# Optimization experiments

Measured on AMD Instinct MI355X. Metric: run time of the kernel, lower is better.

Reference implementation:

```python
import jax, jax.numpy as jnp
import numpy as np

H = 8; DH = 32; MAX_HOP = 256; NUM_EDGE = 25
NHOP = MAX_HOP + 2   # 258 (incl. UNREACHABLE)
NEDGE = NUM_EDGE + 2 # 27  (incl. NO_EDGE)


def _ln(x, g, b, eps=1e-5):
    m = x.mean(-1, keepdims=True)
    v = ((x - m) ** 2).mean(-1, keepdims=True)
    return (x - m) / jnp.sqrt(v + eps) * g + b


def _scatter_bins(att, idx, M):
    # att: [B,H,N,N] probs, idx: [B,N,N] int bins -> [B,H,N,M] scatter-add over keys
    B, Hh, N, _ = att.shape
    idxb = jnp.broadcast_to(idx[:, None, :, :], att.shape)
    bi = jnp.arange(B)[:, None, None, None]
    hi = jnp.arange(Hh)[None, :, None, None]
    ni = jnp.arange(N)[None, None, :, None]
    return jnp.zeros((B, Hh, N, M), att.dtype).at[bi, hi, ni, idxb].add(att)


def _forward(x, mask, distance_mat, edge_attr_mat,
             node_W, node_b, ln1_g, ln1_b, Wq, bq, Wk, bk, Wv, bv, Wo, bo,
             ln2_g, ln2_b, W1, b1, W2, b2,
             q_hop, q_edge, k_hop, k_edge, v_hop, v_edge,
             fln_g, fln_b, out_W, out_b):
    B, N, _ = x.shape
    h = x @ node_W + node_b  # [B,N,DM]
    # index preprocessing (clamp then -1 -> sentinel, as in torch)
    dist = jnp.minimum(distance_mat, MAX_HOP)
    dist = jnp.where(dist == -1, MAX_HOP + 1, dist)
    edge = jnp.minimum(edge_attr_mat, NUM_EDGE)
    edge = jnp.where(edge == -1, NUM_EDGE + 1, edge)

    # ---- encoder layer ----
    y = _ln(h, ln1_g, ln1_b)
    q = (y @ Wq + bq).reshape(B, N, H, DH).transpose(0, 2, 1, 3)  # bhnd
    k = (y @ Wk + bk).reshape(B, N, H, DH).transpose(0, 2, 1, 3)
    v = (y @ Wv + bv).reshape(B, N, H, DH).transpose(0, 2, 1, 3)
    Qh = q_hop.reshape(NHOP, H, DH).transpose(1, 0, 2)   # [H,M,d]
    Qe = q_edge.reshape(NEDGE, H, DH).transpose(1, 0, 2)
    Kh = k_hop.reshape(NHOP, H, DH).transpose(1, 0, 2)
    Ke = k_edge.reshape(NEDGE, H, DH).transpose(1, 0, 2)
    Vh = v_hop.reshape(NHOP, H, DH).transpose(1, 0, 2)
    Ve = v_edge.reshape(NEDGE, H, DH).transpose(1, 0, 2)

    dist_b = jnp.broadcast_to(dist[:, None, :, :], (B, H, N, N))
    edge_b = jnp.broadcast_to(edge[:, None, :, :], (B, H, N, N))

    qh = jnp.einsum('bhnd,hmd->bhnm', q, Qh)  # [B,H,N,M]
    query_hop = jnp.take_along_axis(qh, dist_b, axis=3)
    qe = jnp.einsum('bhnd,hmd->bhnm', q, Qe)
    query_edge = jnp.take_along_axis(qe, edge_b, axis=3)
    kh = jnp.einsum('bhnd,hmd->bhnm', k, Kh)
    # torch gathers along dim 2 of kh^T: key_hop[b,h,i,j] = k_j . Kh[dist[i,j]]
    key_hop = jnp.take_along_axis(jnp.swapaxes(kh, 2, 3), dist_b, axis=2)
    ke = jnp.einsum('bhnd,hmd->bhnm', k, Ke)
    key_edge = jnp.take_along_axis(ke, edge_b, axis=3)

    scale = DH ** (-0.5)
    scores = (jnp.einsum('bhid,bhjd->bhij', q, k)
              + (query_hop + key_hop) + (query_edge + key_edge)) * scale
    scores = jnp.where(mask[:, None, None, :], -jnp.inf, scores)
    att = jax.nn.softmax(scores, axis=-1)

    vha = _scatter_bins(att, dist, NHOP)   # [B,H,N,NHOP]
    vea = _scatter_bins(att, edge, NEDGE)
    ctx = (jnp.einsum('bhij,bhjd->bhid', att, v)
           + jnp.einsum('bhim,hmd->bhid', vha, Vh)
           + jnp.einsum('bhim,hmd->bhid', vea, Ve))
    ctx = ctx.transpose(0, 2, 1, 3).reshape(B, N, H * DH)
    h = h + (ctx @ Wo + bo)

    y = _ln(h, ln2_g, ln2_b)
    y = jax.nn.gelu(y @ W1 + b1, approximate=False) @ W2 + b2
    h = h + y
    # ---- head ----
    out = _ln(h, fln_g, fln_b)
    return out @ out_W + out_b


def setup_inputs() -> dict:
    key = jax.random.key(0)
    ks = jax.random.split(key, 40)
    D_IN, DM, FF, OUT, B, N = 128, 256, 1024, 128, 16, 512
    nrm = lambda k, shape, s=0.02: jax.random.normal(k, shape, jnp.float32) * s
    z = lambda shape: jnp.zeros(shape, jnp.float32)
    o = lambda shape: jnp.ones(shape, jnp.float32)
    return {
        'x': jax.random.normal(ks[0], (B, N, D_IN), jnp.float32),
        'mask': jnp.zeros((B, N), bool),
        'distance_mat': jax.random.randint(ks[1], (B, N, N), 0, 257),
        'edge_attr_mat': jax.random.randint(ks[2], (B, N, N), 0, 26),
        'node_W': nrm(ks[3], (D_IN, DM)), 'node_b': z((DM,)),
        'ln1_g': o((DM,)), 'ln1_b': z((DM,)),
        'Wq': nrm(ks[4], (DM, DM)), 'bq': z((DM,)),
        'Wk': nrm(ks[5], (DM, DM)), 'bk': z((DM,)),
        'Wv': nrm(ks[6], (DM, DM)), 'bv': z((DM,)),
        'Wo': nrm(ks[7], (DM, DM)), 'bo': z((DM,)),
        'ln2_g': o((DM,)), 'ln2_b': z((DM,)),
        'W1': nrm(ks[8], (DM, FF)), 'b1': z((FF,)),
        'W2': nrm(ks[9], (FF, DM)), 'b2': z((DM,)),
        'q_hop': nrm(ks[10], (NHOP, DM)), 'q_edge': nrm(ks[11], (NEDGE, DM)),
        'k_hop': nrm(ks[12], (NHOP, DM)), 'k_edge': nrm(ks[13], (NEDGE, DM)),
        'v_hop': nrm(ks[14], (NHOP, DM)), 'v_edge': nrm(ks[15], (NEDGE, DM)),
        'fln_g': o((DM,)), 'fln_b': z((DM,)),
        'out_W': nrm(ks[16], (DM, OUT)), 'out_b': z((OUT,)),
    }


def reference(x, mask, distance_mat, edge_attr_mat,
              node_W, node_b, ln1_g, ln1_b, Wq, bq, Wk, bk, Wv, bv, Wo, bo,
              ln2_g, ln2_b, W1, b1, W2, b2,
              q_hop, q_edge, k_hop, k_edge, v_hop, v_edge,
              fln_g, fln_b, out_W, out_b):
    return _forward(x, mask, distance_mat, edge_attr_mat,
                    node_W, node_b, ln1_g, ln1_b, Wq, bq, Wk, bk, Wv, bv, Wo, bo,
                    ln2_g, ln2_b, W1, b1, W2, b2,
                    q_hop, q_edge, k_hop, k_edge, v_hop, v_edge,
                    fln_g, fln_b, out_W, out_b)
```

## Files before the change

kernel.cpp:

```cpp
#include <hip/hip_runtime.h>
#include <hip/hip_bf16.h>
#include <math.h>

#define BB 16
#define NN 512
#define DIN 128
#define DM 256
#define NH 8
#define DH 32
#define FF 1024
#define DOUT 128
#define NHOP 258
#define NEDGE 27
#define ROWS (BB*NN)
#define QHE_S 296

typedef short short8 __attribute__((ext_vector_type(8)));
typedef float f32x4 __attribute__((ext_vector_type(4)));

static __device__ __forceinline__ float bf2f(unsigned short u) {
    union { float f; unsigned int i; } c; c.i = ((unsigned int)u) << 16; return c.f;
}
static __device__ __forceinline__ short f2bs(float f) {
    __hip_bfloat16 h = __float2bfloat16(f);
    return *reinterpret_cast<short*>(&h);
}

__global__ __launch_bounds__(256) void k_ln(const float* __restrict__ in, const float* __restrict__ g,
                                            const float* __restrict__ bta, float* __restrict__ out) {
    int row = blockIdx.x * 4 + (threadIdx.x >> 6);
    int l = threadIdx.x & 63;
    float4 xv = ((const float4*)(in + (size_t)row*DM))[l];
    float s = xv.x + xv.y + xv.z + xv.w;
    #pragma unroll
    for (int o = 32; o > 0; o >>= 1) s += __shfl_xor(s, o, 64);
    float mean = s * (1.0f/DM);
    float dx = xv.x-mean, dy = xv.y-mean, dz = xv.z-mean, dw = xv.w-mean;
    float vs = dx*dx + dy*dy + dz*dz + dw*dw;
    #pragma unroll
    for (int o = 32; o > 0; o >>= 1) vs += __shfl_xor(vs, o, 64);
    float r = rsqrtf(vs * (1.0f/DM) + 1e-5f);
    float4 gg = ((const float4*)g)[l];
    float4 bb = ((const float4*)bta)[l];
    float4 ov; ov.x = dx*r*gg.x+bb.x; ov.y = dy*r*gg.y+bb.y; ov.z = dz*r*gg.z+bb.z; ov.w = dw*r*gg.w+bb.w;
    ((float4*)(out + (size_t)row*DM))[l] = ov;
}

template<int K, int N, int ACT, int RES, int QKV>
__global__ __launch_bounds__(256) void k_mgemm(const float* __restrict__ A, const float* __restrict__ W,
                                               const float* __restrict__ bias, float* __restrict__ out) {
    __shared__ __align__(16) short As[64][40];
    __shared__ __align__(16) short Bs[64][40];
    int r0 = blockIdx.x * 64;
    int n0 = blockIdx.y * 64;
    int tid = threadIdx.x;
    int w = tid >> 6, l = tid & 63;

    f32x4 acc[4];
    #pragma unroll
    for (int c = 0; c < 4; ++c) acc[c] = (f32x4){0.f,0.f,0.f,0.f};

    for (int k0 = 0; k0 < K; k0 += 32) {
        __syncthreads();
        {
            int m = tid >> 2, ks = (tid & 3) * 8;
            const float* src = A + (size_t)(r0 + m)*K + k0 + ks;
            float4 f0 = *(const float4*)src;
            float4 f1 = *(const float4*)(src + 4);
            short8 pk;
            pk[0]=f2bs(f0.x); pk[1]=f2bs(f0.y); pk[2]=f2bs(f0.z); pk[3]=f2bs(f0.w);
            pk[4]=f2bs(f1.x); pk[5]=f2bs(f1.y); pk[6]=f2bs(f1.z); pk[7]=f2bs(f1.w);
            *(short8*)&As[m][ks] = pk;
        }
        {
            int n = tid & 63, kg = tid >> 6;
            const float* wp = W + (size_t)(k0 + kg*8)*N + n0 + n;
            short8 pk;
            #pragma unroll
            for (int j = 0; j < 8; ++j) pk[j] = f2bs(wp[(size_t)j*N]);
            *(short8*)&Bs[n][kg*8] = pk;
        }
        __syncthreads();
        short8 af = *(short8*)&As[w*16 + (l & 15)][(l >> 4)*8];
        #pragma unroll
        for (int c = 0; c < 4; ++c) {
            short8 bf = *(short8*)&Bs[c*16 + (l & 15)][(l >> 4)*8];
            acc[c] = __builtin_amdgcn_mfma_f32_16x16x32_bf16(af, bf, acc[c], 0, 0, 0);
        }
    }

    int quad = l >> 4;
    #pragma unroll
    for (int c = 0; c < 4; ++c) {
        int col = n0 + c*16 + (l & 15);
        float bv = bias[col];
        #pragma unroll
        for (int reg = 0; reg < 4; ++reg) {
            int row = r0 + w*16 + quad*4 + reg;
            float val = acc[c][reg] + bv;
            if (ACT) val = 0.5f * val * (1.0f + erff(val * 0.70710678118654752f));
            if (QKV) {
                int b = row >> 9, n = row & (NN-1);
                int hh = col >> 5, d = col & (DH-1);
                out[(size_t)((b*NH + hh)*NN + n)*DH + d] = val;
            } else if (RES) {
                out[(size_t)row*N + col] += val;
            } else {
                out[(size_t)row*N + col] = val;
            }
        }
    }
}

__global__ __launch_bounds__(256) void k_tr(const float* __restrict__ in, float* __restrict__ out, int M) {
    int m = blockIdx.x, t = threadIdx.x;
    out[((size_t)(t >> 5)*M + m)*DH + (t & 31)] = in[(size_t)m*DM + t];
}

__global__ __launch_bounds__(256) void k_trd(const float* __restrict__ in, float* __restrict__ out, int M) {
    int m = blockIdx.x, t = threadIdx.x;
    out[(size_t)t*M + m] = in[(size_t)m*DM + t];
}

__global__ __launch_bounds__(256) void k_tx(const float* __restrict__ k, float* __restrict__ kT) {
    __shared__ float lds[64*33];
    int bh = blockIdx.x;
    int j0 = blockIdx.y * 64;
    int tid = threadIdx.x;
    {
        int jj = tid >> 2, d8 = tid & 3;
        const float* src = k + ((size_t)bh*NN + j0 + jj)*DH + d8*8;
        float4 a = *(const float4*)(src);
        float4 b = *(const float4*)(src + 4);
        float* dst = lds + jj*33 + d8*8;
        dst[0]=a.x; dst[1]=a.y; dst[2]=a.z; dst[3]=a.w;
        dst[4]=b.x; dst[5]=b.y; dst[6]=b.z; dst[7]=b.w;
    }
    __syncthreads();
    {
        int d = tid >> 3, jg = tid & 7;
        float* dst = kT + ((size_t)bh*DH + d)*NN + j0;
        #pragma unroll
        for (int jj2 = 0; jj2 < 8; ++jj2) {
            int j = jg*8 + jj2;
            dst[j] = lds[j*33 + d];
        }
    }
}

__global__ __launch_bounds__(256) void k_kht(const float* __restrict__ kT, const float* __restrict__ k_hop,
                                             __hip_bfloat16* __restrict__ kht) {
    int bm = blockIdx.x;
    int m = bm % NHOP;
    int bh = bm / NHOP;
    int hh = bh & (NH-1);
    float kh[32];
    {
        const float4* khp = (const float4*)(k_hop + (size_t)m*DM + hh*DH);
        #pragma unroll
        for (int c = 0; c < 8; ++c) *(float4*)&kh[c*4] = khp[c];
    }
    const float* kTb = kT + (size_t)bh*DH*NN;
    #pragma unroll
    for (int it = 0; it < 2; ++it) {
        int j = threadIdx.x + it*256;
        float acc = 0.f;
        #pragma unroll
        for (int d = 0; d < DH; ++d) acc += kh[d] * kTb[(size_t)d*NN + j];
        kht[(size_t)bm*NN + j] = __float2bfloat16(acc);
    }
}

__global__ __launch_bounds__(256) void k_qhe(const float* __restrict__ q, const float* __restrict__ k,
                                             const float* __restrict__ Qh_d, const float* __restrict__ Qe_d,
                                             const float* __restrict__ Ke_d, unsigned short* __restrict__ qhe) {
    int bh = blockIdx.x;
    int hh = bh & (NH-1);
    int i0 = blockIdx.y * 16;
    int tid = threadIdx.x;
    __shared__ __align__(16) float As[16][32];
    __shared__ __align__(16) float Ks[16][32];
    {
        int r = (tid & 127) >> 3, c4 = tid & 7;
        const float* src = ((tid < 128) ? q : k) + ((size_t)bh*NN + i0 + r)*DH + c4*4;
        float4 vv = *(const float4*)src;
        float* dst = (tid < 128) ? &As[r][c4*4] : &Ks[r][c4*4];
        *(float4*)dst = vv;
    }
    __syncthreads();
    {
        float acc[16];
        #pragma unroll
        for (int r = 0; r < 16; ++r) acc[r] = 0.f;
        const float* wb = Qh_d + (size_t)hh*32*NHOP + tid;
        for (int d = 0; d < 32; ++d) {
            float wv = wb[(size_t)d*NHOP];
            #pragma unroll
            for (int r = 0; r < 16; ++r) acc[r] += As[r][d] * wv;
        }
        #pragma unroll
        for (int r = 0; r < 16; ++r) {
            __hip_bfloat16 bv = __float2bfloat16(acc[r]);
            qhe[((size_t)bh*NN + i0 + r)*QHE_S + tid] = *(unsigned short*)&bv;
        }
    }
    if (tid < 2) {
        int m = 256 + tid;
        float acc[16];
        #pragma unroll
        for (int r = 0; r < 16; ++r) acc[r] = 0.f;
        const float* wb = Qh_d + (size_t)hh*32*NHOP + m;
        for (int d = 0; d < 32; ++d) {
            float wv = wb[(size_t)d*NHOP];
            #pragma unroll
            for (int r = 0; r < 16; ++r) acc[r] += As[r][d] * wv;
        }
        #pragma unroll
        for (int r = 0; r < 16; ++r) {
            __hip_bfloat16 bv = __float2bfloat16(acc[r]);
            qhe[((size_t)bh*NN + i0 + r)*QHE_S + m] = *(unsigned short*)&bv;
        }
    } else if (tid >= 8 && tid < 8 + NEDGE) {
        int e = tid - 8;
        float acc[16];
        #pragma unroll
        for (int r = 0; r < 16; ++r) acc[r] = 0.f;
        const float* wq = Qe_d + (size_t)hh*32*NEDGE + e;
        const float* wk = Ke_d + (size_t)hh*32*NEDGE + e;
        for (int d = 0; d < 32; ++d) {
            float a = wq[(size_t)d*NEDGE], bbw = wk[(size_t)d*NEDGE];
            #pragma unroll
            for (int r = 0; r < 16; ++r) acc[r] += As[r][d]*a + Ks[r][d]*bbw;
        }
        #pragma unroll
        for (int r = 0; r < 16; ++r) {
            __hip_bfloat16 bv = __float2bfloat16(acc[r]);
            qhe[((size_t)bh*NN + i0 + r)*QHE_S + 264 + e] = *(unsigned short*)&bv;
        }
    }
}

__global__ __launch_bounds__(512) void k_attn(
    const float* __restrict__ q, const float* __restrict__ kT, const float* __restrict__ v,
    const __hip_bfloat16* __restrict__ kht, const int* __restrict__ dist, const int* __restrict__ edge,
    const unsigned char* __restrict__ mask, const unsigned short* __restrict__ qhe,
    const float* __restrict__ Vh_t, const float* __restrict__ Ve_t,
    float* __restrict__ ctx)
{
    int g  = blockIdx.x;
    int rr = g >> 3;
    int b  = (g & 7) + ((rr >> 7) << 3);
    int i0 = (rr & 127) * 4;
    int w  = threadIdx.x >> 6;
    int l  = threadIdx.x & 63;
    int bh = b*NH + w;

    __shared__ unsigned short mje[4][NN];
    __shared__ float qv[NH][4][DH];
    __shared__ __hip_bfloat16 pb[NH][4][NN];
    __shared__ float bins[NH][292];

    {
        int t = threadIdx.x;
        int row = t >> 7, c4 = t & 127;
        int4 dv = ((const int4*)(dist + ((size_t)(b*NN) + i0 + row)*NN))[c4];
        int4 ev = ((const int4*)(edge + ((size_t)(b*NN) + i0 + row)*NN))[c4];
        int m0 = dv.x > 256 ? 256 : dv.x; if (dv.x < 0) m0 = 257;
        int m1 = dv.y > 256 ? 256 : dv.y; if (dv.y < 0) m1 = 257;
        int m2 = dv.z > 256 ? 256 : dv.z; if (dv.z < 0) m2 = 257;
        int m3 = dv.w > 256 ? 256 : dv.w; if (dv.w < 0) m3 = 257;
        int e0 = ev.x > 25 ? 25 : ev.x; if (ev.x < 0) e0 = 26;
        int e1 = ev.y > 25 ? 25 : ev.y; if (ev.y < 0) e1 = 26;
        int e2 = ev.z > 25 ? 25 : ev.z; if (ev.z < 0) e2 = 26;
        int e3 = ev.w > 25 ? 25 : ev.w; if (ev.w < 0) e3 = 26;
        mje[row][c4*4+0] = (unsigned short)(m0 | (e0 << 9));
        mje[row][c4*4+1] = (unsigned short)(m1 | (e1 << 9));
        mje[row][c4*4+2] = (unsigned short)(m2 | (e2 << 9));
        mje[row][c4*4+3] = (unsigned short)(m3 | (e3 << 9));
        #pragma unroll
        for (int rep = 0; rep < 2; ++rep) {
            int i = rep*2 + (l >> 5), d = l & 31;
            qv[w][i][d] = q[((size_t)bh*NN + i0 + i)*DH + d];
        }
        for (int s = l; s < 292; s += 64) bins[w][s] = 0.f;
    }
    __syncthreads();

    float sc[4][8];
    #pragma unroll
    for (int i = 0; i < 4; ++i)
        #pragma unroll
        for (int s = 0; s < 8; ++s) sc[i][s] = 0.f;
    {
        const float* kTb = kT + (size_t)bh*DH*NN;
        for (int d = 0; d < 32; ++d) {
            const float* kr = kTb + (size_t)d*NN + l;
            float k0 = kr[0],   k1 = kr[64],  k2 = kr[128], k3 = kr[192];
            float k4 = kr[256], k5 = kr[320], k6 = kr[384], k7 = kr[448];
            float qa = qv[w][0][d], qb = qv[w][1][d], qc = qv[w][2][d], qd = qv[w][3][d];
            sc[0][0]+=qa*k0; sc[0][1]+=qa*k1; sc[0][2]+=qa*k2; sc[0][3]+=qa*k3;
            sc[0][4]+=qa*k4; sc[0][5]+=qa*k5; sc[0][6]+=qa*k6; sc[0][7]+=qa*k7;
            sc[1][0]+=qb*k0; sc[1][1]+=qb*k1; sc[1][2]+=qb*k2; sc[1][3]+=qb*k3;
            sc[1][4]+=qb*k4; sc[1][5]+=qb*k5; sc[1][6]+=qb*k6; sc[1][7]+=qb*k7;
            sc[2][0]+=qc*k0; sc[2][1]+=qc*k1; sc[2][2]+=qc*k2; sc[2][3]+=qc*k3;
            sc[2][4]+=qc*k4; sc[2][5]+=qc*k5; sc[2][6]+=qc*k6; sc[2][7]+=qc*k7;
            sc[3][0]+=qd*k0; sc[3][1]+=qd*k1; sc[3][2]+=qd*k2; sc[3][3]+=qd*k3;
            sc[3][4]+=qd*k4; sc[3][5]+=qd*k5; sc[3][6]+=qd*k6; sc[3][7]+=qd*k7;
        }
    }

    const __hip_bfloat16* khtb = kht + (size_t)bh*NHOP*NN;
    const unsigned char* mrow = mask + (size_t)b*NN;
    unsigned char msk[8];
    #pragma unroll
    for (int s = 0; s < 8; ++s) msk[s] = mrow[l + 64*s];

    int jc = l >> 3, d4 = l & 7;
    const float* vhb = Vh_t + (size_t)w*NHOP*DH + d4*4;
    const float* veb = Ve_t + (size_t)w*NEDGE*DH + d4*4;
    const float scale = 0.17677669529663687f;
    float4 acc[4];

    #pragma unroll
    for (int i = 0; i < 4; ++i) {
        const unsigned short* qhr = qhe + ((size_t)bh*NN + i0 + i)*QHE_S;
        int mv[8], ev[8];
        #pragma unroll
        for (int s = 0; s < 8; ++s) { int pk = mje[i][l + 64*s]; mv[s] = pk & 511; ev[s] = pk >> 9; }
        unsigned short raw[8];
        #pragma unroll
        for (int s = 0; s < 8; ++s) raw[s] = ((const unsigned short*)khtb)[(size_t)mv[s]*NN + l + 64*s];
        unsigned short qhv[8], qev[8];
        #pragma unroll
        for (int s = 0; s < 8; ++s) qhv[s] = qhr[mv[s]];
        #pragma unroll
        for (int s = 0; s < 8; ++s) qev[s] = qhr[264 + ev[s]];
        float x[8];
        #pragma unroll
        for (int s = 0; s < 8; ++s) {
            float a = (sc[i][s] + bf2f(qhv[s]) + bf2f(raw[s]) + bf2f(qev[s])) * scale;
            if (msk[s]) a = -INFINITY;
            x[s] = a;
        }
        float mx = x[0];
        #pragma unroll
        for (int s = 1; s < 8; ++s) mx = fmaxf(mx, x[s]);
        #pragma unroll
        for (int o = 32; o > 0; o >>= 1) mx = fmaxf(mx, __shfl_xor(mx, o, 64));
        float sum = 0.f;
        #pragma unroll
        for (int s = 0; s < 8; ++s) { x[s] = __expf(x[s] - mx); sum += x[s]; }
        #pragma unroll
        for (int o = 32; o > 0; o >>= 1) sum += __shfl_xor(sum, o, 64);
        float inv = 1.0f / sum;
        #pragma unroll
        for (int s = 0; s < 8; ++s) {
            float ps = x[s] * inv;
            pb[w][i][l + 64*s] = __float2bfloat16(ps);
            atomicAdd(&bins[w][mv[s]], ps);
            atomicAdd(&bins[w][264 + ev[s]], ps);
        }
        float4 a4; a4.x = a4.y = a4.z = a4.w = 0.f;
        for (int t = 0; t < 33; ++t) {
            int m = 8*t + jc;
            if (m < NHOP) {
                float bw = bins[w][m];
                float4 vv = *(const float4*)(vhb + (size_t)m*DH);
                a4.x += bw*vv.x; a4.y += bw*vv.y; a4.z += bw*vv.z; a4.w += bw*vv.w;
            }
        }
        #pragma unroll
        for (int t = 0; t < 4; ++t) {
            int e = 8*t + jc;
            if (e < NEDGE) {
                float bw = bins[w][264 + e];
                float4 vv = *(const float4*)(veb + (size_t)e*DH);
                a4.x += bw*vv.x; a4.y += bw*vv.y; a4.z += bw*vv.z; a4.w += bw*vv.w;
            }
        }
        acc[i] = a4;
        if (i < 3) {
            for (int s2 = l; s2 < 292; s2 += 64) bins[w][s2] = 0.f;
        }
    }

    {
        const float* vb = v + (size_t)bh*NN*DH + d4*4;
        for (int off = 0; off < 64; ++off) {
            int j = 8*off + jc;
            float4 vv = *(const float4*)(vb + (size_t)j*DH);
            #pragma unroll
            for (int i = 0; i < 4; ++i) {
                float p = bf2f(*(const unsigned short*)&pb[w][i][j]);
                acc[i].x += p*vv.x; acc[i].y += p*vv.y; acc[i].z += p*vv.z; acc[i].w += p*vv.w;
            }
        }
    }
    #pragma unroll
    for (int i = 0; i < 4; ++i) {
        #pragma unroll
        for (int o = 8; o <= 32; o <<= 1) {
            acc[i].x += __shfl_xor(acc[i].x, o, 64);
            acc[i].y += __shfl_xor(acc[i].y, o, 64);
            acc[i].z += __shfl_xor(acc[i].z, o, 64);
            acc[i].w += __shfl_xor(acc[i].w, o, 64);
        }
        if (jc == 0) {
            *(float4*)(ctx + ((size_t)b*NN + i0 + i)*DM + w*DH + d4*4) = acc[i];
        }
    }
}

extern "C" void kernel_launch(void* const* d_in, const int* in_sizes, int n_in,
                              void* d_out, int out_size, void* d_ws, size_t ws_size,
                              hipStream_t stream) {
    const float* x     = (const float*)d_in[0];
    const unsigned char* mask = (const unsigned char*)d_in[1];
    const int*   dist  = (const int*)d_in[2];
    const int*   edge  = (const int*)d_in[3];
    const float* node_W = (const float*)d_in[4];
    const float* node_b = (const float*)d_in[5];
    const float* ln1_g = (const float*)d_in[6];
    const float* ln1_b = (const float*)d_in[7];
    const float* Wq = (const float*)d_in[8];
    const float* bq = (const float*)d_in[9];
    const float* Wk = (const float*)d_in[10];
    const float* bk = (const float*)d_in[11];
    const float* Wv = (const float*)d_in[12];
    const float* bv = (const float*)d_in[13];
    const float* Wo = (const float*)d_in[14];
    const float* bo = (const float*)d_in[15];
    const float* ln2_g = (const float*)d_in[16];
    const float* ln2_b = (const float*)d_in[17];
    const float* W1 = (const float*)d_in[18];
    const float* b1 = (const float*)d_in[19];
    const float* W2 = (const float*)d_in[20];
    const float* b2 = (const float*)d_in[21];
    const float* q_hop  = (const float*)d_in[22];
    const float* q_edge = (const float*)d_in[23];
    const float* k_hop  = (const float*)d_in[24];
    const float* k_edge = (const float*)d_in[25];
    const float* v_hop  = (const float*)d_in[26];
    const float* v_edge = (const float*)d_in[27];
    const float* fln_g = (const float*)d_in[28];
    const float* fln_b = (const float*)d_in[29];
    const float* out_W = (const float*)d_in[30];
    const float* out_b = (const float*)d_in[31];
    float* out = (float*)d_out;

    float* ws = (float*)d_ws;
    float* h   = ws + 0;
    float* y   = ws + 2097152;
    float* q   = ws + 4194304;
    float* k   = ws + 6291456;
    float* v   = ws + 8388608;
    float* ctx = ws + 10485760;
    __hip_bfloat16* kht = (__hip_bfloat16*)(ws + 12582912);
    float* ffn = ws + 12582912;
    float* kT  = ws + 21037056;
    unsigned short* qhe = (unsigned short*)(ws + 23134208);
    float* Vh_t = y + 0;
    float* Ve_t = y + 66048;
    float* Qh_d = y + 72960;
    float* Qe_d = y + 139008;
    float* Ke_d = y + 145920;

    k_mgemm<DIN, DM, 0, 0, 0><<<dim3(ROWS/64, DM/64), 256, 0, stream>>>(x, node_W, node_b, h);
    k_ln<<<ROWS/4, 256, 0, stream>>>(h, ln1_g, ln1_b, y);
    k_mgemm<DM, DM, 0, 0, 1><<<dim3(ROWS/64, DM/64), 256, 0, stream>>>(y, Wq, bq, q);
    k_mgemm<DM, DM, 0, 0, 1><<<dim3(ROWS/64, DM/64), 256, 0, stream>>>(y, Wk, bk, k);
    k_mgemm<DM, DM, 0, 0, 1><<<dim3(ROWS/64, DM/64), 256, 0, stream>>>(y, Wv, bv, v);
    k_tr <<<NHOP, 256, 0, stream>>>(v_hop, Vh_t, NHOP);
    k_tr <<<NEDGE, 256, 0, stream>>>(v_edge, Ve_t, NEDGE);
    k_trd<<<NHOP, 256, 0, stream>>>(q_hop, Qh_d, NHOP);
    k_trd<<<NEDGE, 256, 0, stream>>>(q_edge, Qe_d, NEDGE);
    k_trd<<<NEDGE, 256, 0, stream>>>(k_edge, Ke_d, NEDGE);
    k_tx<<<dim3(BB*NH, 8), 256, 0, stream>>>(k, kT);
    k_kht<<<BB*NH*NHOP, 256, 0, stream>>>(kT, k_hop, kht);
    k_qhe<<<dim3(BB*NH, NN/16), 256, 0, stream>>>(q, k, Qh_d, Qe_d, Ke_d, qhe);
    k_attn<<<BB*(NN/4), 512, 0, stream>>>(q, kT, v, kht, dist, edge, mask, qhe,
                                          Vh_t, Ve_t, ctx);
    k_mgemm<DM, DM, 0, 1, 0><<<dim3(ROWS/64, DM/64), 256, 0, stream>>>(ctx, Wo, bo, h);
    k_ln<<<ROWS/4, 256, 0, stream>>>(h, ln2_g, ln2_b, y);
    k_mgemm<DM, FF, 1, 0, 0><<<dim3(ROWS/64, FF/64), 256, 0, stream>>>(y, W1, b1, ffn);
    k_mgemm<FF, DM, 0, 1, 0><<<dim3(ROWS/64, DM/64), 256, 0, stream>>>(ffn, W2, b2, h);
    k_ln<<<ROWS/4, 256, 0, stream>>>(h, fln_g, fln_b, y);
    k_mgemm<DM, DOUT, 0, 0, 0><<<dim3(ROWS/64, DOUT/64), 256, 0, stream>>>(y, out_W, out_b, out);
}
```

Before: 873.2 us.

## Split attention into score kernel and separate bin-value GEMV kernel

The fused attention kernel is split in two. The score kernel now runs 4 heads per 256-thread block instead of 8 heads per 512-thread block, and it writes the per-row hop/edge bin probabilities as bf16 into the qhe buffer, overwriting its now-consumed entries. A new k_av kernel then multiplies those bins by a combined, zero-padded transposed Vh/Ve table and adds the result into ctx. This moves the scattered per-row float4 loads of the hop and edge value tables out of the softmax kernel and cuts its LDS use, at the cost of an extra launch, a global round-trip for the bins, and bf16 rounding of the bin weights.

```diff
diff --git a/kernel.cpp b/kernel.cpp
--- a/kernel.cpp
+++ b/kernel.cpp
@@ -112,14 +112,19 @@
     }
 }
 
-__global__ __launch_bounds__(256) void k_tr(const float* __restrict__ in, float* __restrict__ out, int M) {
-    int m = blockIdx.x, t = threadIdx.x;
-    out[((size_t)(t >> 5)*M + m)*DH + (t & 31)] = in[(size_t)m*DM + t];
-}
-
 __global__ __launch_bounds__(256) void k_trd(const float* __restrict__ in, float* __restrict__ out, int M) {
     int m = blockIdx.x, t = threadIdx.x;
     out[(size_t)t*M + m] = in[(size_t)m*DM + t];
+}
+
+__global__ __launch_bounds__(256) void k_vhve(const float* __restrict__ vh, const float* __restrict__ ve,
+                                              float* __restrict__ out) {
+    int m = blockIdx.x;
+    int t = threadIdx.x;
+    float val = 0.f;
+    if (m < NHOP) val = vh[(size_t)m*DM + t];
+    else if (m >= 264 && m < 264 + NEDGE) val = ve[(size_t)(m - 264)*DM + t];
+    out[((size_t)(t >> 5)*QHE_S + m)*DH + (t & 31)] = val;
 }
 
 __global__ __launch_bounds__(256) void k_tx(const float* __restrict__ k, float* __restrict__ kT) {
@@ -199,10 +204,8 @@
             for (int r = 0; r < 16; ++r) acc[r] += As[r][d] * wv;
         }
         #pragma unroll
-        for (int r = 0; r < 16; ++r) {
-            __hip_bfloat16 bv = __float2bfloat16(acc[r]);
-            qhe[((size_t)bh*NN + i0 + r)*QHE_S + tid] = *(unsigned short*)&bv;
-        }
+        for (int r = 0; r < 16; ++r)
+            qhe[((size_t)bh*NN + i0 + r)*QHE_S + tid] = (unsigned short)f2bs(acc[r]);
     }
     if (tid < 2) {
         int m = 256 + tid;
@@ -216,10 +219,8 @@
             for (int r = 0; r < 16; ++r) acc[r] += As[r][d] * wv;
         }
         #pragma unroll
-        for (int r = 0; r < 16; ++r) {
-            __hip_bfloat16 bv = __float2bfloat16(acc[r]);
-            qhe[((size_t)bh*NN + i0 + r)*QHE_S + m] = *(unsigned short*)&bv;
-        }
+        for (int r = 0; r < 16; ++r)
+            qhe[((size_t)bh*NN + i0 + r)*QHE_S + m] = (unsigned short)f2bs(acc[r]);
     } else if (tid >= 8 && tid < 8 + NEDGE) {
         int e = tid - 8;
         float acc[16];
@@ -233,50 +234,54 @@
             for (int r = 0; r < 16; ++r) acc[r] += As[r][d]*a + Ks[r][d]*bbw;
         }
         #pragma unroll
-        for (int r = 0; r < 16; ++r) {
-            __hip_bfloat16 bv = __float2bfloat16(acc[r]);
-            qhe[((size_t)bh*NN + i0 + r)*QHE_S + 264 + e] = *(unsigned short*)&bv;
-        }
-    }
-}
-
-__global__ __launch_bounds__(512) void k_attn(
+        for (int r = 0; r < 16; ++r)
+            qhe[((size_t)bh*NN + i0 + r)*QHE_S + 264 + e] = (unsigned short)f2bs(acc[r]);
+    }
+}
+
+__global__ __launch_bounds__(256) void k_score(
     const float* __restrict__ q, const float* __restrict__ kT, const float* __restrict__ v,
     const __hip_bfloat16* __restrict__ kht, const int* __restrict__ dist, const int* __restrict__ edge,
-    const unsigned char* __restrict__ mask, const unsigned short* __restrict__ qhe,
-    const float* __restrict__ Vh_t, const float* __restrict__ Ve_t,
+    const unsigned char* __restrict__ mask, unsigned short* __restrict__ qhe,
     float* __restrict__ ctx)
 {
-    int g  = blockIdx.x;
-    int rr = g >> 3;
-    int b  = (g & 7) + ((rr >> 7) << 3);
-    int i0 = (rr & 127) * 4;
-    int w  = threadIdx.x >> 6;
-    int l  = threadIdx.x & 63;
-    int bh = b*NH + w;
+    int g   = blockIdx.x;
+    int r   = g >> 3;
+    int b   = (g & 7) + ((r >> 8) << 3);
+    int rem = r & 255;
+    int i0  = (rem >> 1) * 4;
+    int hg  = rem & 1;
+    int w   = threadIdx.x >> 6;
+    int l   = threadIdx.x & 63;
+    int hh  = hg*4 + w;
+    int bh  = b*NH + hh;
 
     __shared__ unsigned short mje[4][NN];
-    __shared__ float qv[NH][4][DH];
-    __shared__ __hip_bfloat16 pb[NH][4][NN];
-    __shared__ float bins[NH][292];
+    __shared__ float qv[4][4][DH];
+    __shared__ __hip_bfloat16 pb[4][4][NN];
+    __shared__ float bins[4][292];
 
     {
         int t = threadIdx.x;
-        int row = t >> 7, c4 = t & 127;
-        int4 dv = ((const int4*)(dist + ((size_t)(b*NN) + i0 + row)*NN))[c4];
-        int4 ev = ((const int4*)(edge + ((size_t)(b*NN) + i0 + row)*NN))[c4];
-        int m0 = dv.x > 256 ? 256 : dv.x; if (dv.x < 0) m0 = 257;
-        int m1 = dv.y > 256 ? 256 : dv.y; if (dv.y < 0) m1 = 257;
-        int m2 = dv.z > 256 ? 256 : dv.z; if (dv.z < 0) m2 = 257;
-        int m3 = dv.w > 256 ? 256 : dv.w; if (dv.w < 0) m3 = 257;
-        int e0 = ev.x > 25 ? 25 : ev.x; if (ev.x < 0) e0 = 26;
-        int e1 = ev.y > 25 ? 25 : ev.y; if (ev.y < 0) e1 = 26;
-        int e2 = ev.z > 25 ? 25 : ev.z; if (ev.z < 0) e2 = 26;
-        int e3 = ev.w > 25 ? 25 : ev.w; if (ev.w < 0) e3 = 26;
-        mje[row][c4*4+0] = (unsigned short)(m0 | (e0 << 9));
-        mje[row][c4*4+1] = (unsigned short)(m1 | (e1 << 9));
-        mje[row][c4*4+2] = (unsigned short)(m2 | (e2 << 9));
-        mje[row][c4*4+3] = (unsigned short)(m3 | (e3 << 9));
+        int row = t >> 6, c0 = t & 63;
+        #pragma unroll
+        for (int rep = 0; rep < 2; ++rep) {
+            int c4 = c0 + rep*64;
+            int4 dv = ((const int4*)(dist + ((size_t)(b*NN) + i0 + row)*NN))[c4];
+            int4 ev = ((const int4*)(edge + ((size_t)(b*NN) + i0 + row)*NN))[c4];
+            int m0 = dv.x > 256 ? 256 : dv.x; if (dv.x < 0) m0 = 257;
+            int m1 = dv.y > 256 ? 256 : dv.y; if (dv.y < 0) m1 = 257;
+            int m2 = dv.z > 256 ? 256 : dv.z; if (dv.z < 0) m2 = 257;
+            int m3 = dv.w > 256 ? 256 : dv.w; if (dv.w < 0) m3 = 257;
+            int e0 = ev.x > 25 ? 25 : ev.x; if (ev.x < 0) e0 = 26;
+            int e1 = ev.y > 25 ? 25 : ev.y; if (ev.y < 0) e1 = 26;
+            int e2 = ev.z > 25 ? 25 : ev.z; if (ev.z < 0) e2 = 26;
+            int e3 = ev.w > 25 ? 25 : ev.w; if (ev.w < 0) e3 = 26;
+            mje[row][c4*4+0] = (unsigned short)(m0 | (e0 << 9));
+            mje[row][c4*4+1] = (unsigned short)(m1 | (e1 << 9));
+            mje[row][c4*4+2] = (unsigned short)(m2 | (e2 << 9));
+            mje[row][c4*4+3] = (unsigned short)(m3 | (e3 << 9));
+        }
         #pragma unroll
         for (int rep = 0; rep < 2; ++rep) {
             int i = rep*2 + (l >> 5), d = l & 31;
@@ -314,27 +319,23 @@
     unsigned char msk[8];
     #pragma unroll
     for (int s = 0; s < 8; ++s) msk[s] = mrow[l + 64*s];
-
-    int jc = l >> 3, d4 = l & 7;
-    const float* vhb = Vh_t + (size_t)w*NHOP*DH + d4*4;
-    const float* veb = Ve_t + (size_t)w*NEDGE*DH + d4*4;
     const float scale = 0.17677669529663687f;
-    float4 acc[4];
 
     #pragma unroll
     for (int i = 0; i < 4; ++i) {
-        const unsigned short* qhr = qhe + ((size_t)bh*NN + i0 + i)*QHE_S;
-        int mv[8], ev[8];
-        #pragma unroll
-        for (int s = 0; s < 8; ++s) { int pk = mje[i][l + 64*s]; mv[s] = pk & 511; ev[s] = pk >> 9; }
+        unsigned short* qhr = qhe + ((size_t)bh*NN + i0 + i)*QHE_S;
+        int pk[8];
+        #pragma unroll
+        for (int s = 0; s < 8; ++s) pk[s] = mje[i][l + 64*s];
         unsigned short raw[8];
         #pragma unroll
-        for (int s = 0; s < 8; ++s) raw[s] = ((const unsigned short*)khtb)[(size_t)mv[s]*NN + l + 64*s];
+        for (int s = 0; s < 8; ++s)
+            raw[s] = ((const unsigned short*)khtb)[(size_t)(pk[s] & 511)*NN + l + 64*s];
         unsigned short qhv[8], qev[8];
         #pragma unroll
-        for (int s = 0; s < 8; ++s) qhv[s] = qhr[mv[s]];
-        #pragma unroll
-        for (int s = 0; s < 8; ++s) qev[s] = qhr[264 + ev[s]];
+        for (int s = 0; s < 8; ++s) qhv[s] = qhr[pk[s] & 511];
+        #pragma unroll
+        for (int s = 0; s < 8; ++s) qev[s] = qhr[264 + (pk[s] >> 9)];
         float x[8];
         #pragma unroll
         for (int s = 0; s < 8; ++s) {
@@ -357,33 +358,23 @@
         for (int s = 0; s < 8; ++s) {
             float ps = x[s] * inv;
             pb[w][i][l + 64*s] = __float2bfloat16(ps);
-            atomicAdd(&bins[w][mv[s]], ps);
-            atomicAdd(&bins[w][264 + ev[s]], ps);
-        }
-        float4 a4; a4.x = a4.y = a4.z = a4.w = 0.f;
-        for (int t = 0; t < 33; ++t) {
-            int m = 8*t + jc;
-            if (m < NHOP) {
-                float bw = bins[w][m];
-                float4 vv = *(const float4*)(vhb + (size_t)m*DH);
-                a4.x += bw*vv.x; a4.y += bw*vv.y; a4.z += bw*vv.z; a4.w += bw*vv.w;
+            atomicAdd(&bins[w][pk[s] & 511], ps);
+            atomicAdd(&bins[w][264 + (pk[s] >> 9)], ps);
+        }
+        #pragma unroll
+        for (int s5 = 0; s5 < 5; ++s5) {
+            int idx = l + 64*s5;
+            if (idx < 292) {
+                qhr[idx] = (unsigned short)f2bs(bins[w][idx]);
+                if (i < 3) bins[w][idx] = 0.f;
             }
         }
-        #pragma unroll
-        for (int t = 0; t < 4; ++t) {
-            int e = 8*t + jc;
-            if (e < NEDGE) {
-                float bw = bins[w][264 + e];
-                float4 vv = *(const float4*)(veb + (size_t)e*DH);
-                a4.x += bw*vv.x; a4.y += bw*vv.y; a4.z += bw*vv.z; a4.w += bw*vv.w;
-            }
-        }
-        acc[i] = a4;
-        if (i < 3) {
-            for (int s2 = l; s2 < 292; s2 += 64) bins[w][s2] = 0.f;
-        }
-    }
-
+    }
+
+    int jc = l >> 3, d4 = l & 7;
+    float4 acc[4];
+    #pragma unroll
+    for (int i = 0; i < 4; ++i) { acc[i].x = acc[i].y = acc[i].z = acc[i].w = 0.f; }
     {
         const float* vb = v + (size_t)bh*NN*DH + d4*4;
         for (int off = 0; off < 64; ++off) {
@@ -406,9 +397,33 @@
             acc[i].w += __shfl_xor(acc[i].w, o, 64);
         }
         if (jc == 0) {
-            *(float4*)(ctx + ((size_t)b*NN + i0 + i)*DM + w*DH + d4*4) = acc[i];
-        }
-    }
+            *(float4*)(ctx + ((size_t)b*NN + i0 + i)*DM + hh*DH + d4*4) = acc[i];
+        }
+    }
+}
+
+__global__ __launch_bounds__(512) void k_av(const unsigned short* __restrict__ vha,
+                                            const float* __restrict__ vhve, float* __restrict__ ctx) {
+    int bh = blockIdx.x;
+    int hh = bh & (NH-1);
+    int b  = bh >> 3;
+    int i0 = blockIdx.y * 16;
+    __shared__ unsigned short lds[16*QHE_S];
+    int tid = threadIdx.x;
+    for (int idx = tid; idx < 16*QHE_S; idx += 512) {
+        int rr = idx / QHE_S, c = idx - rr*QHE_S;
+        lds[idx] = vha[((size_t)bh*NN + i0 + rr)*QHE_S + c];
+    }
+    __syncthreads();
+    int i = tid >> 5, d = tid & 31;
+    const float* tb = vhve + (size_t)hh*QHE_S*DH + d;
+    const unsigned short* pr = &lds[i*QHE_S];
+    float acc = 0.f;
+    #pragma unroll 4
+    for (int m = 0; m < 292; ++m) {
+        acc += bf2f(pr[m]) * tb[(size_t)m*DH];
+    }
+    ctx[((size_t)b*NN + i0 + i)*DM + hh*DH + d] += acc;
 }
 
 extern "C" void kernel_launch(void* const* d_in, const int* in_sizes, int n_in,
@@ -459,27 +474,25 @@
     float* ffn = ws + 12582912;
     float* kT  = ws + 21037056;
     unsigned short* qhe = (unsigned short*)(ws + 23134208);
-    float* Vh_t = y + 0;
-    float* Ve_t = y + 66048;
-    float* Qh_d = y + 72960;
-    float* Qe_d = y + 139008;
-    float* Ke_d = y + 145920;
+    float* Qh_d = y + 0;
+    float* Qe_d = y + 66048;
+    float* Ke_d = y + 72960;
+    float* vhve = y + 81920;
 
     k_mgemm<DIN, DM, 0, 0, 0><<<dim3(ROWS/64, DM/64), 256, 0, stream>>>(x, node_W, node_b, h);
     k_ln<<<ROWS/4, 256, 0, stream>>>(h, ln1_g, ln1_b, y);
     k_mgemm<DM, DM, 0, 0, 1><<<dim3(ROWS/64, DM/64), 256, 0, stream>>>(y, Wq, bq, q);
     k_mgemm<DM, DM, 0, 0, 1><<<dim3(ROWS/64, DM/64), 256, 0, stream>>>(y, Wk, bk, k);
     k_mgemm<DM, DM, 0, 0, 1><<<dim3(ROWS/64, DM/64), 256, 0, stream>>>(y, Wv, bv, v);
-    k_tr <<<NHOP, 256, 0, stream>>>(v_hop, Vh_t, NHOP);
-    k_tr <<<NEDGE, 256, 0, stream>>>(v_edge, Ve_t, NEDGE);
     k_trd<<<NHOP, 256, 0, stream>>>(q_hop, Qh_d, NHOP);
     k_trd<<<NEDGE, 256, 0, stream>>>(q_edge, Qe_d, NEDGE);
     k_trd<<<NEDGE, 256, 0, stream>>>(k_edge, Ke_d, NEDGE);
+    k_vhve<<<QHE_S, 256, 0, stream>>>(v_hop, v_edge, vhve);
     k_tx<<<dim3(BB*NH, 8), 256, 0, stream>>>(k, kT);
     k_kht<<<BB*NH*NHOP, 256, 0, stream>>>(kT, k_hop, kht);
     k_qhe<<<dim3(BB*NH, NN/16), 256, 0, stream>>>(q, k, Qh_d, Qe_d, Ke_d, qhe);
-    k_attn<<<BB*(NN/4), 512, 0, stream>>>(q, kT, v, kht, dist, edge, mask, qhe,
-                                          Vh_t, Ve_t, ctx);
+    k_score<<<BB*(NN/4)*2, 256, 0, stream>>>(q, kT, v, kht, dist, edge, mask, qhe, ctx);
+    k_av<<<dim3(BB*NH, NN/16), 512, 0, stream>>>(qhe, vhve, ctx);
     k_mgemm<DM, DM, 0, 1, 0><<<dim3(ROWS/64, DM/64), 256, 0, stream>>>(ctx, Wo, bo, h);
     k_ln<<<ROWS/4, 256, 0, stream>>>(h, ln2_g, ln2_b, y);
     k_mgemm<DM, FF, 1, 0, 0><<<dim3(ROWS/64, FF/64), 256, 0, stream>>>(y, W1, b1, ffn);
```

After: 866.5 us. No clear change (-0.8%).
